# Performance work log

Measured on AMD Instinct MI355X. Metric: run time of the kernel, lower is better.

The kernel has to match this reference:

```python
import jax, jax.numpy as jnp
import numpy as np

N_NODES = 100000
N_EDGES = 800000
NUM_FEATURES = 81
NUM_BOND = 22
OUT_CHANNEL = 64
D_COORD = 3  # 'distance' rule applies to feature indices [0:3]


def setup_inputs() -> dict:
    key = jax.random.key(0)
    k1, k2, k3, k4, k5, k6 = jax.random.split(key, 6)
    features = jax.random.normal(k1, (N_NODES, NUM_FEATURES), dtype=jnp.float32)
    bond = jax.random.normal(k2, (N_EDGES, NUM_BOND), dtype=jnp.float32)
    w_s = jax.random.normal(k3, (NUM_FEATURES, OUT_CHANNEL), dtype=jnp.float32) * 0.1
    w_n = jax.random.normal(k4, (NUM_FEATURES + NUM_BOND, OUT_CHANNEL), dtype=jnp.float32) * 0.1
    src = jax.random.randint(k5, (N_EDGES,), 0, N_NODES)
    dst = jax.random.randint(k6, (N_EDGES,), 0, N_NODES)
    return {"features": features, "bond": bond, "w_s": w_s, "w_n": w_n,
            "src": src, "dst": dst}


def reference(features, bond, w_s, w_n, src, dst):
    # Gather endpoint features per edge: [E, F]
    self_f = features[src]
    nbr_f = features[dst]

    # Rule 1: 'distance' on [0:3] -> keep neighbour coords, compute L2 distance
    diff = self_f[:, :D_COORD] - nbr_f[:, :D_COORD]
    dist = jnp.sqrt(jnp.sum(diff * diff, axis=-1))      # [E]
    d = jnp.where(dist > 0, dist, jnp.float32(0.01))

    # Rule 2 (last, single-index): 'sum' on [3:]
    seg1 = nbr_f[:, :D_COORD]                           # [E, 3]
    seg2 = self_f[:, D_COORD:] + nbr_f[:, D_COORD:]     # [E, 78]

    # Distance normalization applies to the whole combined vector (pre-bond)
    combined = jnp.concatenate([seg1, seg2], axis=-1) / (d * d)[:, None]
    edge_vec = jnp.concatenate([combined, bond], axis=-1)  # [E, F + B]

    contrib = edge_vec @ w_n                            # [E, out]
    agg = jax.ops.segment_sum(contrib, src, num_segments=features.shape[0])
    return features @ w_s + agg                         # [N, out]
```

## Files before the change

kernel.cpp:

```cpp
#include <hip/hip_runtime.h>

#define N_NODES 100000
#define N_EDGES 800000
#define NF 81
#define NB 22
#define OC 64
#define SCAN_CHUNK 1024
#define SCAN_BLOCKS ((N_NODES + SCAN_CHUNK - 1) / SCAN_CHUNK)

typedef __attribute__((ext_vector_type(8))) short bf16x8;
typedef __attribute__((ext_vector_type(4))) float f32x4;

#if defined(__has_builtin)
#if __has_builtin(__builtin_amdgcn_fdot2_f32_bf16)
#define HAVE_FDOT2 1
#endif
#endif

#ifdef HAVE_FDOT2
typedef __attribute__((ext_vector_type(2))) __bf16 bfv2;
#endif

__device__ inline float dot2b(unsigned a, unsigned b, float c) {
#ifdef HAVE_FDOT2
    return __builtin_amdgcn_fdot2_f32_bf16(__builtin_bit_cast(bfv2, a),
                                           __builtin_bit_cast(bfv2, b), c, false);
#else
    return c + __uint_as_float(a << 16)         * __uint_as_float(b << 16)
             + __uint_as_float(a & 0xffff0000u) * __uint_as_float(b & 0xffff0000u);
#endif
}

__device__ inline unsigned short bfsplit(float v, float& rest) {
    const unsigned b = __float_as_uint(v);
    const unsigned short h = (unsigned short)((b + 0x7fffu + ((b >> 16) & 1u)) >> 16);
    rest = v - __uint_as_float(((unsigned)h) << 16);
    return h;
}

__device__ inline unsigned pk_bf16(float a, float b) {
    const unsigned ua = (__float_as_uint(a) + 0x8000u) >> 16;
    const unsigned ub = (__float_as_uint(b) + 0x8000u) & 0xffff0000u;
    return ua | ub;
}

__device__ inline int clampe(int p) {
    return ((unsigned)p < (unsigned)N_EDGES) ? p : 0;
}

__global__ void k_wprep(const float* __restrict__ w_s, const float* __restrict__ w_n,
                        short* __restrict__ bt)
{
    const int tid = blockIdx.x * blockDim.x + threadIdx.x;
    if (tid >= 128 * 96) return;
    const int c = tid / 96;
    const int k = tid - c * 96;
    float v = 0.f;
    if (k < NF) v = (c < OC) ? w_s[k * OC + c] : w_n[k * OC + (c - OC)];
    float rest, dummy;
    const unsigned short h = bfsplit(v, rest);
    const unsigned short l = bfsplit(rest, dummy);
    bt[c * 96 + k]               = (short)h;
    bt[128 * 96 + c * 96 + k]    = (short)l;
}

__global__ __launch_bounds__(256) void k_node_mfma(
    const float* __restrict__ feat, const short* __restrict__ bt,
    float* __restrict__ out, float* __restrict__ pb, float4* __restrict__ xyz)
{
    __shared__ short shA[2 * 64 * 104];
    const int t    = threadIdx.x;
    const int lane = t & 63;
    const int w    = t >> 6;
    const int n0   = blockIdx.x * 64;

    const int krow = (lane >> 4) * 8;
    bf16x8 Bh[3][2], Bl[3][2];
#pragma unroll
    for (int kt = 0; kt < 3; ++kt)
#pragma unroll
        for (int c = 0; c < 2; ++c) {
            const int col = w * 32 + c * 16 + (lane & 15);
            const int off = col * 96 + kt * 32 + krow;
            Bh[kt][c] = *(const bf16x8*)(bt + off);
            Bl[kt][c] = *(const bf16x8*)(bt + 128 * 96 + off);
        }

    const long gbase = (long)n0 * NF;
    const long gmax  = (long)N_NODES * NF;
    for (int j = t; j < (64 * NF) / 4; j += 256) {
        const int flat = j * 4;
        float v[4];
        if (gbase + flat + 3 < gmax) {
            const float4 q = *(const float4*)(feat + gbase + flat);
            v[0] = q.x; v[1] = q.y; v[2] = q.z; v[3] = q.w;
        } else {
#pragma unroll
            for (int i = 0; i < 4; ++i)
                v[i] = (gbase + flat + i < gmax) ? feat[gbase + flat + i] : 0.f;
        }
#pragma unroll
        for (int i = 0; i < 4; ++i) {
            const int fi  = flat + i;
            const int row = (int)((unsigned)fi / 81u);
            const int k   = fi - row * 81;
            float rest, dummy;
            const unsigned short h = bfsplit(v[i], rest);
            const unsigned short l = bfsplit(rest, dummy);
            shA[row * 104 + k]        = (short)h;
            shA[6656 + row * 104 + k] = (short)l;
        }
    }
    for (int j = t; j < 64 * 16; j += 256) {
        const int row = j >> 4, k = NF + (j & 15);
        shA[row * 104 + k] = 0;
        shA[6656 + row * 104 + k] = 0;
    }

    if (t < 64 && n0 + t < N_NODES) {
        const float* fp = feat + (long)(n0 + t) * NF;
        xyz[n0 + t] = make_float4(fp[0], fp[1], fp[2], 0.f);
    }
    __syncthreads();

    f32x4 acc[4][2];
#pragma unroll
    for (int rt = 0; rt < 4; ++rt)
#pragma unroll
        for (int c = 0; c < 2; ++c)
            acc[rt][c] = (f32x4){0.f, 0.f, 0.f, 0.f};

#pragma unroll
    for (int kt = 0; kt < 3; ++kt) {
        bf16x8 Ah[4], Al[4];
#pragma unroll
        for (int rt = 0; rt < 4; ++rt) {
            const int o = (rt * 16 + (lane & 15)) * 104 + kt * 32 + krow;
            Ah[rt] = *(const bf16x8*)(shA + o);
            Al[rt] = *(const bf16x8*)(shA + 6656 + o);
        }
#pragma unroll
        for (int rt = 0; rt < 4; ++rt)
#pragma unroll
            for (int c = 0; c < 2; ++c) {
                f32x4 a = acc[rt][c];
                a = __builtin_amdgcn_mfma_f32_16x16x32_bf16(Ah[rt], Bh[kt][c], a, 0, 0, 0);
                a = __builtin_amdgcn_mfma_f32_16x16x32_bf16(Ah[rt], Bl[kt][c], a, 0, 0, 0);
                a = __builtin_amdgcn_mfma_f32_16x16x32_bf16(Al[rt], Bh[kt][c], a, 0, 0, 0);
                acc[rt][c] = a;
            }
    }

    const int c0    = w * 32 + (lane & 15);
    float* db       = (w < 2) ? out : pb;
    const int cbase = (w < 2) ? c0 : c0 - OC;
    const int r0    = (lane >> 4) * 4;
#pragma unroll
    for (int rt = 0; rt < 4; ++rt)
#pragma unroll
        for (int c = 0; c < 2; ++c)
#pragma unroll
            for (int reg = 0; reg < 4; ++reg) {
                const int node = n0 + rt * 16 + r0 + reg;
                if (node < N_NODES)
                    db[(long)node * OC + cbase + c * 16] = acc[rt][c][reg];
            }
}

__global__ void k_hist(const int* __restrict__ src, int* __restrict__ cnt,
                       int* __restrict__ rank) {
    const int e = blockIdx.x * blockDim.x + threadIdx.x;
    if (e < N_EDGES) rank[e] = atomicAdd(&cnt[src[e]], 1);
}

__global__ __launch_bounds__(256) void k_scan_blk(
    const int* __restrict__ cnt, int* __restrict__ row, int* __restrict__ bsum)
{
    __shared__ int sh[256];
    const int t = threadIdx.x;
    const int base = blockIdx.x * SCAN_CHUNK + t * 4;
    int c0 = 0, c1 = 0, c2 = 0, c3 = 0;
    if (base + 3 < N_NODES) {
        const int4 c = *(const int4*)(cnt + base);
        c0 = c.x; c1 = c.y; c2 = c.z; c3 = c.w;
    } else {
        if (base + 0 < N_NODES) c0 = cnt[base + 0];
        if (base + 1 < N_NODES) c1 = cnt[base + 1];
        if (base + 2 < N_NODES) c2 = cnt[base + 2];
    }
    const int s = c0 + c1 + c2 + c3;
    sh[t] = s;
    __syncthreads();
    for (int off = 1; off < 256; off <<= 1) {
        int v = sh[t];
        int a = (t >= off) ? sh[t - off] : 0;
        __syncthreads();
        sh[t] = v + a;
        __syncthreads();
    }
    const int excl = sh[t] - s;
    if (t == 255) bsum[blockIdx.x] = sh[255];
    if (base + 3 < N_NODES) {
        int4 r;
        r.x = excl; r.y = excl + c0; r.z = excl + c0 + c1; r.w = excl + c0 + c1 + c2;
        *(int4*)(row + base) = r;
    } else {
        int e = excl;
        if (base + 0 < N_NODES) { row[base + 0] = e; e += c0; }
        if (base + 1 < N_NODES) { row[base + 1] = e; e += c1; }
        if (base + 2 < N_NODES) { row[base + 2] = e; }
    }
}

__global__ void k_scan_top(int* __restrict__ bsum, int* __restrict__ row) {
    __shared__ int sh[128];
    const int t = threadIdx.x;
    const int v = (t < SCAN_BLOCKS) ? bsum[t] : 0;
    sh[t] = v;
    __syncthreads();
    for (int off = 1; off < 128; off <<= 1) {
        int x = sh[t];
        int a = (t >= off) ? sh[t - off] : 0;
        __syncthreads();
        sh[t] = x + a;
        __syncthreads();
    }
    if (t < SCAN_BLOCKS) bsum[t] = sh[t] - v;
    if (t == 127) row[N_NODES] = sh[127];
}

__global__ __launch_bounds__(256) void k_scan_add(
    int* __restrict__ row, const int* __restrict__ bsum)
{
    const int off = bsum[blockIdx.x];
    const int base = blockIdx.x * SCAN_CHUNK + threadIdx.x * 4;
    if (base + 3 < N_NODES) {
        int4 r = *(const int4*)(row + base);
        r.x += off; r.y += off; r.z += off; r.w += off;
        *(int4*)(row + base) = r;
    } else {
#pragma unroll
        for (int k = 0; k < 4; ++k)
            if (base + k < N_NODES)
                row[base + k] += off;
    }
}

__global__ void k_perm(const int* __restrict__ src, const int* __restrict__ rank,
                       const int* __restrict__ row, int* __restrict__ perm) {
    const int e = blockIdx.x * blockDim.x + threadIdx.x;
    if (e < N_EDGES) perm[row[src[e]] + rank[e]] = e;
}

__global__ void k_prep8(const int* __restrict__ src, const int* __restrict__ dst,
                        const float4* __restrict__ xyz, uint2* __restrict__ rec8)
{
    const int e = blockIdx.x * blockDim.x + threadIdx.x;
    if (e >= N_EDGES) return;
    const int s = src[e];
    const int d = dst[e];
    const float4 a = xyz[s], b = xyz[d];
    const float dx = a.x - b.x, dy = a.y - b.y, dz = a.z - b.z;
    const float d2 = dx * dx + dy * dy + dz * dz;
    const float inv = (d2 > 0.f) ? __builtin_amdgcn_rcpf(d2) : 1.0e4f;
    rec8[e] = make_uint2(__float_as_uint(inv), (unsigned)d);
}

__global__ __launch_bounds__(256) void k_bsum(
    const int* __restrict__ row, const int* __restrict__ perm,
    const float* __restrict__ bond, unsigned* __restrict__ bs)
{
    const int lane = threadIdx.x & 63;
    const int wid  = (int)((blockIdx.x * blockDim.x + threadIdx.x) >> 6);
    if (wid >= N_NODES) return;
    const int n = __builtin_amdgcn_readfirstlane(wid);
    const int rs = row[n], re = row[n + 1];

    float sx = 0.f, sy = 0.f;
    int i = rs;
    for (; i + 4 <= re; i += 4) {
        int pe[4];
#pragma unroll
        for (int u = 0; u < 4; ++u)
            pe[u] = __builtin_amdgcn_readfirstlane(clampe(perm[i + u]));
        if (lane < 11) {
            float2 v[4];
#pragma unroll
            for (int u = 0; u < 4; ++u)
                v[u] = *(const float2*)(bond + (size_t)pe[u] * NB + 2 * lane);
#pragma unroll
            for (int u = 0; u < 4; ++u) { sx += v[u].x; sy += v[u].y; }
        }
    }
    for (; i < re; ++i) {
        const int pe = __builtin_amdgcn_readfirstlane(clampe(perm[i]));
        if (lane < 11) {
            const float2 v = *(const float2*)(bond + (size_t)pe * NB + 2 * lane);
            sx += v.x; sy += v.y;
        }
    }
    if (lane < 11)
        bs[n * 12 + lane] = pk_bf16(sx, sy);
}

__global__ __launch_bounds__(256) void k_gather(
    const int* __restrict__ row, const int* __restrict__ perm,
    const uint2* __restrict__ rec8, const unsigned* __restrict__ bs,
    const float* __restrict__ w_n, const float* __restrict__ pb,
    const float4* __restrict__ xyz, float* __restrict__ out)
{
    const int lane = threadIdx.x & 63;
    const int wid  = (int)((blockIdx.x * blockDim.x + threadIdx.x) >> 6);
    if (wid >= N_NODES) return;
    const int n = __builtin_amdgcn_readfirstlane(wid);

    unsigned wp[11];
#pragma unroll
    for (int j = 0; j < 11; ++j)
        wp[j] = pk_bf16(w_n[(NF + 2 * j) * OC + lane],
                        w_n[(NF + 2 * j + 1) * OC + lane]);
    const float w0 = w_n[0 * OC + lane];
    const float w1 = w_n[1 * OC + lane];
    const float w2 = w_n[2 * OC + lane];

    const int rs = row[n], re = row[n + 1];
    const float4 xs = xyz[n];
    const float pa = pb[(long)n * OC + lane]
                   - (xs.x * w0 + xs.y * w1 + xs.z * w2);

    float acc = 0.f;
    float inv_sum = 0.f;
    int i = rs;

    for (; i + 8 <= re; i += 8) {
        int pe[8];
#pragma unroll
        for (int u = 0; u < 8; ++u)
            pe[u] = __builtin_amdgcn_readfirstlane(clampe(perm[i + u]));
        uint2 r[8];
#pragma unroll
        for (int u = 0; u < 8; ++u) r[u] = rec8[pe[u]];
        float pbt[8];
#pragma unroll
        for (int u = 0; u < 8; ++u)
            pbt[u] = pb[(long)(int)r[u].y * OC + lane];
#pragma unroll
        for (int u = 0; u < 8; ++u) {
            const float inv = __uint_as_float(r[u].x);
            acc += inv * pbt[u];
            inv_sum += inv;
        }
    }
    for (; i < re; ++i) {
        const int pe = __builtin_amdgcn_readfirstlane(clampe(perm[i]));
        const uint2 r = rec8[pe];
        const float inv = __uint_as_float(r.x);
        acc += inv * pb[(long)(int)r.y * OC + lane];
        inv_sum += inv;
    }
    acc += pa * inv_sum;

    const unsigned* bsn = bs + n * 12;
    float bc = 0.f;
#pragma unroll
    for (int j = 0; j < 11; ++j)
        bc = dot2b(bsn[j], wp[j], bc);

    out[(long)n * OC + lane] += acc + bc;
}

extern "C" void kernel_launch(void* const* d_in, const int* in_sizes, int n_in,
                              void* d_out, int out_size, void* d_ws, size_t ws_size,
                              hipStream_t stream) {
    const float* feat = (const float*)d_in[0];
    const float* bond = (const float*)d_in[1];
    const float* w_s  = (const float*)d_in[2];
    const float* w_n  = (const float*)d_in[3];
    const int*   src  = (const int*)d_in[4];
    const int*   dstv = (const int*)d_in[5];
    float* out = (float*)d_out;

    char* base = (char*)d_ws;
    float*    pb     = (float*)   (base);
    float4*   xyz    = (float4*)  (base + 25600000);
    int*      row    = (int*)     (base + 27200000);
    int*      cnt    = (int*)     (base + 27600016);
    int*      rank   = (int*)     (base + 28000016);
    int*      bsc    = (int*)     (base + 31200016);
    short*    btw    = (short*)   (base + 31200640);
    uint2*    rec8   = (uint2*)   (base + 31249792);
    int*      perm   = (int*)     (base + 37649792);
    unsigned* bsv    = (unsigned*)(base + 40849792);

    hipMemsetAsync(cnt, 0, N_NODES * sizeof(int), stream);

    k_wprep   <<<48, 256, 0, stream>>>(w_s, w_n, btw);
    k_node_mfma<<<(N_NODES + 63) / 64, 256, 0, stream>>>(feat, btw, out, pb, xyz);
    k_hist    <<<(N_EDGES + 255) / 256, 256, 0, stream>>>(src, cnt, rank);
    k_scan_blk<<<SCAN_BLOCKS, 256, 0, stream>>>(cnt, row, bsc);
    k_scan_top<<<1, 128, 0, stream>>>(bsc, row);
    k_scan_add<<<SCAN_BLOCKS, 256, 0, stream>>>(row, bsc);
    k_perm    <<<(N_EDGES + 255) / 256, 256, 0, stream>>>(src, rank, row, perm);
    k_prep8   <<<(N_EDGES + 255) / 256, 256, 0, stream>>>(src, dstv, xyz, rec8);
    k_bsum    <<<(N_NODES * 64 + 255) / 256, 256, 0, stream>>>(row, perm, bond, bsv);
    k_gather  <<<(N_NODES * 64 + 255) / 256, 256, 0, stream>>>(row, perm, rec8,
                                                               bsv, w_n, pb,
                                                               xyz, out);
}
```

Measured before the change: 334.1 us.

## Store per-edge records in CSR-sorted order and split bond sums across half-waves

The per-edge record kernel now walks the permutation and writes distance-inverse and destination records in CSR order. The gather kernel can then stream them contiguously instead of doing an indirect perm lookup plus a random record read per edge. The bond-sum kernel now uses both 32-lane halves of the wavefront to load two edges' bond rows at once, then combines them with shuffles. The extra indirection moves into the record-building kernel, whose src/dst reads become scattered, and a 4-wide tail loop is added to the gather.

```diff
diff --git a/kernel.cpp b/kernel.cpp
--- a/kernel.cpp
+++ b/kernel.cpp
@@ -252,18 +252,20 @@
     if (e < N_EDGES) perm[row[src[e]] + rank[e]] = e;
 }
 
-__global__ void k_prep8(const int* __restrict__ src, const int* __restrict__ dst,
-                        const float4* __restrict__ xyz, uint2* __restrict__ rec8)
-{
-    const int e = blockIdx.x * blockDim.x + threadIdx.x;
-    if (e >= N_EDGES) return;
+__global__ void k_sortrec(const int* __restrict__ perm, const int* __restrict__ src,
+                          const int* __restrict__ dst, const float4* __restrict__ xyz,
+                          uint2* __restrict__ rec8s)
+{
+    const int i = blockIdx.x * blockDim.x + threadIdx.x;
+    if (i >= N_EDGES) return;
+    const int e = clampe(perm[i]);
     const int s = src[e];
     const int d = dst[e];
     const float4 a = xyz[s], b = xyz[d];
     const float dx = a.x - b.x, dy = a.y - b.y, dz = a.z - b.z;
     const float d2 = dx * dx + dy * dy + dz * dz;
     const float inv = (d2 > 0.f) ? __builtin_amdgcn_rcpf(d2) : 1.0e4f;
-    rec8[e] = make_uint2(__float_as_uint(inv), (unsigned)d);
+    rec8s[i] = make_uint2(__float_as_uint(inv), (unsigned)d);
 }
 
 __global__ __launch_bounds__(256) void k_bsum(
@@ -276,38 +278,49 @@
     const int n = __builtin_amdgcn_readfirstlane(wid);
     const int rs = row[n], re = row[n + 1];
 
-    float sx = 0.f, sy = 0.f;
+    const int h = lane >> 5;
+    const int c = lane & 31;
+
+    float s = 0.f;
     int i = rs;
-    for (; i + 4 <= re; i += 4) {
-        int pe[4];
-#pragma unroll
-        for (int u = 0; u < 4; ++u)
-            pe[u] = __builtin_amdgcn_readfirstlane(clampe(perm[i + u]));
-        if (lane < 11) {
-            float2 v[4];
+    for (; i + 8 <= re; i += 8) {
+        int pes[8];
+#pragma unroll
+        for (int u = 0; u < 8; ++u)
+            pes[u] = __builtin_amdgcn_readfirstlane(clampe(perm[i + u]));
+        if (c < 22) {
+            float v[4];
 #pragma unroll
             for (int u = 0; u < 4; ++u)
-                v[u] = *(const float2*)(bond + (size_t)pe[u] * NB + 2 * lane);
-#pragma unroll
-            for (int u = 0; u < 4; ++u) { sx += v[u].x; sy += v[u].y; }
-        }
-    }
-    for (; i < re; ++i) {
+                v[u] = bond[(size_t)pes[2 * u + h] * NB + c];
+#pragma unroll
+            for (int u = 0; u < 4; ++u) s += v[u];
+        }
+    }
+    for (; i + 2 <= re; i += 2) {
+        const int peA = __builtin_amdgcn_readfirstlane(clampe(perm[i]));
+        const int peB = __builtin_amdgcn_readfirstlane(clampe(perm[i + 1]));
+        if (c < 22)
+            s += bond[(size_t)(h ? peB : peA) * NB + c];
+    }
+    if (i < re) {
         const int pe = __builtin_amdgcn_readfirstlane(clampe(perm[i]));
-        if (lane < 11) {
-            const float2 v = *(const float2*)(bond + (size_t)pe * NB + 2 * lane);
-            sx += v.x; sy += v.y;
-        }
-    }
+        if (h == 0 && c < 22)
+            s += bond[(size_t)pe * NB + c];
+    }
+
+    const float st = s + __shfl_xor(s, 32);
+    const float a = __shfl(st, 2 * lane);
+    const float b = __shfl(st, 2 * lane + 1);
     if (lane < 11)
-        bs[n * 12 + lane] = pk_bf16(sx, sy);
+        bs[n * 12 + lane] = pk_bf16(a, b);
 }
 
 __global__ __launch_bounds__(256) void k_gather(
-    const int* __restrict__ row, const int* __restrict__ perm,
-    const uint2* __restrict__ rec8, const unsigned* __restrict__ bs,
-    const float* __restrict__ w_n, const float* __restrict__ pb,
-    const float4* __restrict__ xyz, float* __restrict__ out)
+    const int* __restrict__ row, const uint2* __restrict__ rec8s,
+    const unsigned* __restrict__ bs, const float* __restrict__ w_n,
+    const float* __restrict__ pb, const float4* __restrict__ xyz,
+    float* __restrict__ out)
 {
     const int lane = threadIdx.x & 63;
     const int wid  = (int)((blockIdx.x * blockDim.x + threadIdx.x) >> 6);
@@ -330,16 +343,14 @@
 
     float acc = 0.f;
     float inv_sum = 0.f;
-    int i = rs;
-
-    for (; i + 8 <= re; i += 8) {
-        int pe[8];
-#pragma unroll
-        for (int u = 0; u < 8; ++u)
-            pe[u] = __builtin_amdgcn_readfirstlane(clampe(perm[i + u]));
+    const uint2* rp = rec8s + rs;
+    const int m = re - rs;
+    int i = 0;
+
+    for (; i + 8 <= m; i += 8) {
         uint2 r[8];
 #pragma unroll
-        for (int u = 0; u < 8; ++u) r[u] = rec8[pe[u]];
+        for (int u = 0; u < 8; ++u) r[u] = rp[i + u];
         float pbt[8];
 #pragma unroll
         for (int u = 0; u < 8; ++u)
@@ -351,9 +362,23 @@
             inv_sum += inv;
         }
     }
-    for (; i < re; ++i) {
-        const int pe = __builtin_amdgcn_readfirstlane(clampe(perm[i]));
-        const uint2 r = rec8[pe];
+    for (; i + 4 <= m; i += 4) {
+        uint2 r[4];
+#pragma unroll
+        for (int u = 0; u < 4; ++u) r[u] = rp[i + u];
+        float pbt[4];
+#pragma unroll
+        for (int u = 0; u < 4; ++u)
+            pbt[u] = pb[(long)(int)r[u].y * OC + lane];
+#pragma unroll
+        for (int u = 0; u < 4; ++u) {
+            const float inv = __uint_as_float(r[u].x);
+            acc += inv * pbt[u];
+            inv_sum += inv;
+        }
+    }
+    for (; i < m; ++i) {
+        const uint2 r = rp[i];
         const float inv = __uint_as_float(r.x);
         acc += inv * pb[(long)(int)r.y * OC + lane];
         inv_sum += inv;
@@ -388,7 +413,7 @@
     int*      rank   = (int*)     (base + 28000016);
     int*      bsc    = (int*)     (base + 31200016);
     short*    btw    = (short*)   (base + 31200640);
-    uint2*    rec8   = (uint2*)   (base + 31249792);
+    uint2*    rec8s  = (uint2*)   (base + 31249792);
     int*      perm   = (int*)     (base + 37649792);
     unsigned* bsv    = (unsigned*)(base + 40849792);
 
@@ -401,9 +426,9 @@
     k_scan_top<<<1, 128, 0, stream>>>(bsc, row);
     k_scan_add<<<SCAN_BLOCKS, 256, 0, stream>>>(row, bsc);
     k_perm    <<<(N_EDGES + 255) / 256, 256, 0, stream>>>(src, rank, row, perm);
-    k_prep8   <<<(N_EDGES + 255) / 256, 256, 0, stream>>>(src, dstv, xyz, rec8);
+    k_sortrec <<<(N_EDGES + 255) / 256, 256, 0, stream>>>(perm, src, dstv, xyz,
+                                                          rec8s);
     k_bsum    <<<(N_NODES * 64 + 255) / 256, 256, 0, stream>>>(row, perm, bond, bsv);
-    k_gather  <<<(N_NODES * 64 + 255) / 256, 256, 0, stream>>>(row, perm, rec8,
-                                                               bsv, w_n, pb,
-                                                               xyz, out);
-}
+    k_gather  <<<(N_NODES * 64 + 255) / 256, 256, 0, stream>>>(row, rec8s, bsv,
+                                                               w_n, pb, xyz, out);
+}
```

Measured after the change: 313.8 us. 1.06x faster.
